# Optimization experiments

Hardware: AMD Instinct MI355X
Metric: run time of the kernel (lower is better)

Reference implementation:

```python
import jax, jax.numpy as jnp
import numpy as np

SEQ = 2048
DIM = 2048
GROUPS = 8
GROUP_SIZE = 4
DQK = DIM // (GROUPS * GROUP_SIZE)  # 64 (also dim_v)


def _glorot(key, shape):
    # Faithful to source: dim_in = prod(shape[-1]) == shape[-1], so sigma = 1/sqrt(shape[-1])
    sigma = np.sqrt(2.0 / (shape[-1] + shape[-1])).astype(np.float32)
    return jax.random.normal(key, shape, dtype=jnp.float32) * sigma


def rope(x):
    """RoPE on last axis; x: [..., seq, dim]. Closed-form per-pair rotation."""
    seq, dim = x.shape[-2], x.shape[-1]
    half = dim // 2
    # angle[s, j] = s * 10000^(-2j/dim)
    inv_freq = 10000.0 ** (-2.0 * jnp.arange(half, dtype=jnp.float32) / dim)
    ang = jnp.arange(seq, dtype=jnp.float32)[:, None] * inv_freq[None, :]  # [seq, half]
    c, s = jnp.cos(ang), jnp.sin(ang)
    xp = x.reshape(*x.shape[:-1], half, 2)
    x1, x2 = xp[..., 0], xp[..., 1]
    out = jnp.stack([c * x1 - s * x2, s * x1 + c * x2], axis=-1)
    return out.reshape(x.shape)


def setup_inputs() -> dict:
    key = jax.random.key(0)
    kx, kq, kk, kv, ko = jax.random.split(key, 5)
    return {
        "x": jax.random.normal(kx, (SEQ, DIM), dtype=jnp.float32),
        "w_query": _glorot(kq, (GROUPS, GROUP_SIZE, DIM, DQK)),
        "w_key": _glorot(kk, (GROUPS, DIM, DQK)),
        "w_value": _glorot(kv, (GROUPS, DIM, DQK)),
        "w_out": _glorot(ko, (GROUPS, GROUP_SIZE, DQK, DIM)),
    }


def reference(x, w_query, w_key, w_value, w_out):
    seq = x.shape[0]
    dqk = w_query.shape[-1]
    # projections: g=groups, h=group_size (query heads per group)
    q = rope(jnp.einsum('sd,ghdk->ghsk', x, w_query))  # [g,h,seq,dqk]
    k = rope(jnp.einsum('sd,gdk->gsk', x, w_key))      # [g,seq,dqk]
    v = jnp.einsum('sd,gdv->gsv', x, w_value)          # [g,seq,dv]
    scores = jnp.einsum('ghsk,gtk->ghst', q, k) / jnp.sqrt(jnp.float32(dqk))
    causal = jnp.tril(jnp.ones((seq, seq), dtype=bool))  # log(tril(ones)) == 0 / -inf
    scores = jnp.where(causal, scores, -jnp.inf)
    probs = jax.nn.softmax(scores, axis=-1)
    o = jnp.einsum('ghst,gtv->ghsv', probs, v)
    # per-head out-proj then sum over (g, h)
    return jnp.einsum('ghsv,ghvd->sd', o, w_out)
```

## Files before the change

### kernel.cpp

```cpp
#include <hip/hip_runtime.h>
#include <hip/hip_bf16.h>

#define SEQ 2048
#define DIMM 2048
#define NQH 32
#define NKVH 8
#define HD 64

typedef _Float16 half8 __attribute__((ext_vector_type(8)));
typedef float f32x4 __attribute__((ext_vector_type(4)));
typedef __fp16 fp16raw2 __attribute__((ext_vector_type(2)));
using fp16 = _Float16;

typedef __attribute__((address_space(1))) unsigned int ga_u32;
typedef __attribute__((address_space(3))) unsigned int ls_u32;

__device__ __forceinline__ void gll16(const void* g, void* l) {
    __builtin_amdgcn_global_load_lds((const ga_u32*)g, (ls_u32*)l, 16, 0, 0);
}

__global__ void prep_kernel(const float* __restrict__ x,
                            const float* __restrict__ wq, const float* __restrict__ wk,
                            const float* __restrict__ wv, const float* __restrict__ wo,
                            fp16* __restrict__ xh, fp16* __restrict__ wqkvt,
                            fp16* __restrict__ w2t) {
    __shared__ float tile[64][65];
    const int bx = blockIdx.x;
    const int t = threadIdx.x;
    if (bx < 1024) {
#pragma unroll
        for (int it = 0; it < 4; it++) {
            int i = bx * 4096 + it * 1024 + t * 4;
            float4 v = *reinterpret_cast<const float4*>(x + i);
            fp16* o = xh + i;
            o[0] = (fp16)v.x; o[1] = (fp16)v.y; o[2] = (fp16)v.z; o[3] = (fp16)v.w;
        }
    } else if (bx < 2560) {
        const int zi = bx - 1024;
        const int z = zi >> 5;
        const int r0 = (zi & 31) * 64;
        const float* inh = (z < 32) ? wq + (size_t)z * SEQ * HD
                                    : (z < 40) ? wk + (size_t)(z - 32) * SEQ * HD
                                               : wv + (size_t)(z - 40) * SEQ * HD;
        fp16* outh = wqkvt + (size_t)z * HD * SEQ;
#pragma unroll
        for (int i = 0; i < 16; i++) {
            int idx = i * 256 + t;
            int r = idx >> 6, c = idx & 63;
            tile[r][c] = inh[(size_t)(r0 + r) * HD + c];
        }
        __syncthreads();
#pragma unroll
        for (int i = 0; i < 16; i++) {
            int idx = i * 256 + t;
            int cc = idx >> 6, rr = idx & 63;
            outh[(size_t)cc * SEQ + r0 + rr] = (fp16)tile[rr][cc];
        }
    } else {
        const int zi = bx - 2560;
        const int r0 = (zi >> 5) * 64, c0 = (zi & 31) * 64;
#pragma unroll
        for (int i = 0; i < 16; i++) {
            int idx = i * 256 + t;
            int r = idx >> 6, c = idx & 63;
            tile[r][c] = wo[(size_t)(r0 + r) * 2048 + c0 + c];
        }
        __syncthreads();
#pragma unroll
        for (int i = 0; i < 16; i++) {
            int idx = i * 256 + t;
            int cc = idx >> 6, rr = idx & 63;
            w2t[(size_t)(c0 + cc) * 2048 + r0 + rr] = (fp16)tile[rr][cc];
        }
    }
}

__global__ void rope_vt_kernel(const fp16* __restrict__ proj, fp16* __restrict__ qb,
                               fp16* __restrict__ kb, fp16* __restrict__ vtb) {
    __shared__ fp16 tile[64][72];
    const int bx = blockIdx.x;
    if (bx < 10240) {
        int tid = bx * 256 + threadIdx.x;
        int pair = tid & 31;
        int s = (tid >> 5) & 2047;
        int head = tid >> 16;
        const fp16* src = proj + (size_t)s * 3072 + head * HD + 2 * pair;
        float x1 = (float)src[0];
        float x2 = (float)src[1];
        float invf = expf(-((float)pair / 32.0f) * 9.210340371976184f);
        float ang = (float)s * invf;
        float sn, cs;
        sincosf(ang, &sn, &cs);
        float o1 = cs * x1 - sn * x2;
        float o2 = sn * x1 + cs * x2;
        fp16* dst;
        if (head < NQH) {
            o1 *= 0.18033688011112042f;
            o2 *= 0.18033688011112042f;
            dst = qb + ((size_t)head * SEQ + s) * HD + 2 * pair;
        } else {
            dst = kb + ((size_t)(head - NQH) * SEQ + s) * HD + 2 * pair;
        }
        dst[0] = (fp16)o1;
        dst[1] = (fp16)o2;
    } else {
        const int idx = bx - 10240;
        const int g = idx >> 5;
        const int s0 = (idx & 31) * 64;
        const int t = threadIdx.x;
#pragma unroll
        for (int i = 0; i < 16; i++) {
            int id2 = i * 256 + t;
            int r = id2 >> 6, c = id2 & 63;
            tile[r][c] = proj[(size_t)(s0 + r) * 3072 + 2560 + g * HD + c];
        }
        __syncthreads();
#pragma unroll
        for (int i = 0; i < 16; i++) {
            int id2 = i * 256 + t;
            int cc = id2 >> 6, rr = id2 & 63;
            vtb[((size_t)g * HD + cc) * SEQ + s0 + rr] = tile[rr][cc];
        }
    }
}

template <int BM, int BN, int WF32>
__global__ __launch_bounds__(256) void gemm_tpl(
    const fp16* __restrict__ A, const fp16* __restrict__ Bt, void* __restrict__ Cout, int Nout) {
    __shared__ fp16 As[2][BM][64];
    __shared__ fp16 Bs[2][BN][64];
    const int t = threadIdx.x;
    const int m0 = blockIdx.x * BM, n0 = blockIdx.y * BN;
    const int wid = t >> 6, lane = t & 63;
    const int wm = (wid >> 1) * (BM / 2), wn = (wid & 1) * (BN / 2);
    const int lr = lane & 15, lg = lane >> 4;
    constexpr int MR = BM / 32, NR = BN / 32;
    f32x4 acc[MR][NR] = {};
    auto stage_ = [&](int kt, int b) {
#pragma unroll
        for (int s = t; s < BM * 8; s += 256) {
            int row = s >> 3, ch = s & 7;
            int lch = ch ^ (row & 7);
            gll16(A + (size_t)(m0 + row) * 2048 + (kt << 6) + lch * 8,
                  (char*)&As[b][0][0] + s * 16);
        }
#pragma unroll
        for (int s = t; s < BN * 8; s += 256) {
            int row = s >> 3, ch = s & 7;
            int lch = ch ^ (row & 7);
            gll16(Bt + (size_t)(n0 + row) * 2048 + (kt << 6) + lch * 8,
                  (char*)&Bs[b][0][0] + s * 16);
        }
    };
    stage_(0, 0);
    __syncthreads();
    for (int kt = 0; kt < 32; ++kt) {
        const int cur = kt & 1;
        if (kt + 1 < 32) stage_(kt + 1, cur ^ 1);
#pragma unroll
        for (int kk = 0; kk < 2; kk++) {
            half8 af[MR], bfv[NR];
#pragma unroll
            for (int m = 0; m < MR; m++) {
                int row = wm + m * 16 + lr;
                af[m] = *(const half8*)((const char*)&As[cur][row][0] +
                                        (((kk * 4 + lg) ^ (row & 7)) * 16));
            }
#pragma unroll
            for (int n = 0; n < NR; n++) {
                int row = wn + n * 16 + lr;
                bfv[n] = *(const half8*)((const char*)&Bs[cur][row][0] +
                                         (((kk * 4 + lg) ^ (row & 7)) * 16));
            }
            __builtin_amdgcn_s_setprio(1);
#pragma unroll
            for (int m = 0; m < MR; m++)
#pragma unroll
                for (int n = 0; n < NR; n++)
                    acc[m][n] = __builtin_amdgcn_mfma_f32_16x16x32_f16(af[m], bfv[n], acc[m][n], 0, 0, 0);
            __builtin_amdgcn_s_setprio(0);
        }
        __syncthreads();
    }
#pragma unroll
    for (int m = 0; m < MR; m++)
#pragma unroll
        for (int n = 0; n < NR; n++)
#pragma unroll
            for (int r = 0; r < 4; r++) {
                int row = m0 + wm + m * 16 + lg * 4 + r;
                int col = n0 + wn + n * 16 + lr;
                if (WF32)
                    ((float*)Cout)[(size_t)row * Nout + col] = acc[m][n][r];
                else
                    ((fp16*)Cout)[(size_t)row * Nout + col] = (fp16)acc[m][n][r];
            }
}

__global__ __launch_bounds__(256) void attn_kernel(
    const fp16* __restrict__ qb, const fp16* __restrict__ kb,
    const fp16* __restrict__ vt, fp16* __restrict__ o_all) {
    __shared__ fp16 Kb[2][64][64];
    __shared__ fp16 Vb[2][64][64];
    __shared__ fp16 P[4][16][64];
    const int t = threadIdx.x, wid = t >> 6, lane = t & 63;
    const int bx = blockIdx.x;
    const int grp = bx >> 5;
    const int a = grp & 7;
    const int sel = grp >> 3;
    const int qt = (sel == 0) ? (31 - a) : (sel == 1) ? (8 + a) : (sel == 2) ? (23 - a) : a;
    const int head = bx & 31;
    const int g = head >> 2;
    const int lr = lane & 15, lg = lane >> 4;
    const fp16* qh = qb + (size_t)head * SEQ * HD;
    const fp16* kh = kb + (size_t)g * SEQ * HD;
    const fp16* vh = vt + (size_t)g * HD * SEQ;
    const int srow = lane >> 3, schunk = lane & 7;
    const int qr0 = qt * 64 + wid * 16;
    char* pb = (char*)&P[wid][0][0];

    half8 aq0 = *reinterpret_cast<const half8*>(qh + (size_t)(qr0 + lr) * HD + lg * 8);
    half8 aq1 = *reinterpret_cast<const half8*>(qh + (size_t)(qr0 + lr) * HD + 32 + lg * 8);
    f32x4 o[4] = {};
    float m_ = -1e30f, lsum_ = 0.0f;
    const int nt = qt + 1;

    auto stage = [&](int kt, int b) {
        const int kv0 = kt << 6;
#pragma unroll
        for (int i = 0; i < 2; ++i) {
            int row = wid * 16 + i * 8 + srow;
            int sw = (schunk ^ srow) * 8;
            gll16(kh + (size_t)(kv0 + row) * HD + sw, &Kb[b][wid * 16 + i * 8][0]);
            gll16(vh + (size_t)row * SEQ + kv0 + sw, &Vb[b][wid * 16 + i * 8][0]);
        }
    };

    stage(0, 0);
    __syncthreads();
    for (int tt = 0; tt < nt; ++tt) {
        const int cur = tt & 1;
        if (tt + 1 < nt) stage(tt + 1, cur ^ 1);
        const int kv0 = tt << 6;
        f32x4 sc[4];
        __builtin_amdgcn_s_setprio(1);
#pragma unroll
        for (int f = 0; f < 4; ++f) {
            int row = f * 16 + lr;
            const char* kbp = (const char*)&Kb[cur][row][0];
            half8 b0 = *(const half8*)(kbp + (((lg) ^ (row & 7)) * 16));
            half8 b1 = *(const half8*)(kbp + (((4 + lg) ^ (row & 7)) * 16));
            f32x4 s = {};
            s = __builtin_amdgcn_mfma_f32_16x16x32_f16(b0, aq0, s, 0, 0, 0);
            s = __builtin_amdgcn_mfma_f32_16x16x32_f16(b1, aq1, s, 0, 0, 0);
            sc[f] = s;
        }
        __builtin_amdgcn_s_setprio(0);
        if (tt == qt) {
            const int q = qr0 + lr;
#pragma unroll
            for (int f = 0; f < 4; f++)
#pragma unroll
                for (int r = 0; r < 4; r++) {
                    int kv = kv0 + f * 16 + lg * 4 + r;
                    if (kv > q) sc[f][r] = -1e30f;
                }
        }
        float lmax = sc[0][0];
#pragma unroll
        for (int f = 0; f < 4; f++)
#pragma unroll
            for (int r = 0; r < 4; r++) lmax = fmaxf(lmax, sc[f][r]);
        if (!__all(lmax <= m_ + 11.0f)) {
            float v = lmax;
            v = fmaxf(v, __shfl_xor(v, 16));
            v = fmaxf(v, __shfl_xor(v, 32));
            float mn = fmaxf(m_, v);
            float alpha = exp2f(m_ - mn);
            m_ = mn;
            lsum_ *= alpha;
            float al[4];
#pragma unroll
            for (int r = 0; r < 4; r++) al[r] = __shfl(alpha, lg * 4 + r);
#pragma unroll
            for (int vf = 0; vf < 4; vf++)
#pragma unroll
                for (int r = 0; r < 4; r++) o[vf][r] *= al[r];
        }
#pragma unroll
        for (int f = 0; f < 4; f++) {
            float p0 = exp2f(sc[f][0] - m_);
            float p1 = exp2f(sc[f][1] - m_);
            float p2 = exp2f(sc[f][2] - m_);
            float p3 = exp2f(sc[f][3] - m_);
            lsum_ += (p0 + p1) + (p2 + p3);
            fp16raw2 k0 = __builtin_amdgcn_cvt_pkrtz(p0, p1);
            fp16raw2 k1 = __builtin_amdgcn_cvt_pkrtz(p2, p3);
            uint2 w;
            w.x = __builtin_bit_cast(unsigned int, k0);
            w.y = __builtin_bit_cast(unsigned int, k1);
            *(uint2*)(pb + lr * 128 + ((f * 32 + lg * 8) ^ ((lr & 7) << 4))) = w;
        }
        __builtin_amdgcn_s_setprio(1);
#pragma unroll
        for (int h = 0; h < 2; h++) {
            half8 pa = *(const half8*)(pb + lr * 128 + (((h * 4 + lg) ^ (lr & 7)) * 16));
#pragma unroll
            for (int vf = 0; vf < 4; vf++) {
                int d = vf * 16 + lr;
                int xo = ((h * 4 + lg) ^ (d & 7)) * 16;
                half8 bv = *(const half8*)((const char*)&Vb[cur][d][0] + xo);
                o[vf] = __builtin_amdgcn_mfma_f32_16x16x32_f16(pa, bv, o[vf], 0, 0, 0);
            }
        }
        __builtin_amdgcn_s_setprio(0);
        __syncthreads();
    }
    lsum_ += __shfl_xor(lsum_, 16);
    lsum_ += __shfl_xor(lsum_, 32);
    float li[4];
#pragma unroll
    for (int r = 0; r < 4; r++) li[r] = 1.0f / __shfl(lsum_, lg * 4 + r);
#pragma unroll
    for (int vf = 0; vf < 4; vf++)
#pragma unroll
        for (int r = 0; r < 4; r++) {
            float v = o[vf][r] * li[r];
            o_all[(size_t)(qr0 + lg * 4 + r) * 2048 + head * 64 + vf * 16 + lr] = (fp16)v;
        }
}

extern "C" void kernel_launch(void* const* d_in, const int* in_sizes, int n_in,
                              void* d_out, int out_size, void* d_ws, size_t ws_size,
                              hipStream_t stream) {
    const float* x  = (const float*)d_in[0];
    const float* wq = (const float*)d_in[1];
    const float* wk = (const float*)d_in[2];
    const float* wv = (const float*)d_in[3];
    const float* wo = (const float*)d_in[4];
    float* out = (float*)d_out;
    char* ws = (char*)d_ws;

    fp16* xh    = (fp16*)(ws);
    fp16* wqkvt = (fp16*)(ws + ((size_t)8 << 20));
    fp16* proj  = (fp16*)(ws + ((size_t)20 << 20));
    fp16* o_all = proj;
    fp16* w2t   = (fp16*)(ws + ((size_t)32 << 20));
    fp16* qbuf  = (fp16*)(ws + ((size_t)40 << 20));
    fp16* kbuf  = (fp16*)(ws + ((size_t)48 << 20));
    fp16* vtb   = (fp16*)(ws + ((size_t)50 << 20));

    prep_kernel<<<dim3(3584), 256, 0, stream>>>(x, wq, wk, wv, wo, xh, wqkvt, w2t);
    gemm_tpl<64, 128, 0><<<dim3(32, 24), 256, 0, stream>>>(xh, wqkvt, proj, 3072);
    rope_vt_kernel<<<dim3(10496), 256, 0, stream>>>(proj, qbuf, kbuf, vtb);
    attn_kernel<<<dim3(1024), 256, 0, stream>>>(qbuf, kbuf, vtb, o_all);
    gemm_tpl<64, 128, 1><<<dim3(32, 16), 256, 0, stream>>>(o_all, w2t, out, 2048);
}
```

Baseline: 133.8 us.

## Fuse RoPE, Q scaling and V transpose into the QKV projection GEMM epilogue

Replaces the separate QKV GEMM plus rope/transpose kernel with one GEMM whose epilogue applies RoPE (using a lane shuffle to get the paired element), the query scale, and an LDS-staged transpose of V written straight into the attention input buffers. This removes one kernel launch and the round trip of the intermediate projection buffer through global memory. The cost is per-element sincos work in the GEMM epilogue and scattered 2-byte stores for Q/K.

```diff
diff --git a/kernel.cpp b/kernel.cpp
--- a/kernel.cpp
+++ b/kernel.cpp
@@ -75,51 +75,106 @@
     }
 }
 
-__global__ void rope_vt_kernel(const fp16* __restrict__ proj, fp16* __restrict__ qb,
-                               fp16* __restrict__ kb, fp16* __restrict__ vtb) {
-    __shared__ fp16 tile[64][72];
-    const int bx = blockIdx.x;
-    if (bx < 10240) {
-        int tid = bx * 256 + threadIdx.x;
-        int pair = tid & 31;
-        int s = (tid >> 5) & 2047;
-        int head = tid >> 16;
-        const fp16* src = proj + (size_t)s * 3072 + head * HD + 2 * pair;
-        float x1 = (float)src[0];
-        float x2 = (float)src[1];
-        float invf = expf(-((float)pair / 32.0f) * 9.210340371976184f);
-        float ang = (float)s * invf;
-        float sn, cs;
-        sincosf(ang, &sn, &cs);
-        float o1 = cs * x1 - sn * x2;
-        float o2 = sn * x1 + cs * x2;
-        fp16* dst;
-        if (head < NQH) {
-            o1 *= 0.18033688011112042f;
-            o2 *= 0.18033688011112042f;
-            dst = qb + ((size_t)head * SEQ + s) * HD + 2 * pair;
-        } else {
-            dst = kb + ((size_t)(head - NQH) * SEQ + s) * HD + 2 * pair;
-        }
-        dst[0] = (fp16)o1;
-        dst[1] = (fp16)o2;
+__global__ __launch_bounds__(256) void gemm_qkv_fused(
+    const fp16* __restrict__ A, const fp16* __restrict__ Bt,
+    fp16* __restrict__ qb, fp16* __restrict__ kb, fp16* __restrict__ vtb) {
+    __shared__ fp16 As[2][64][64];
+    __shared__ fp16 Bs[2][128][64];
+    const int t = threadIdx.x;
+    const int m0 = blockIdx.x * 64, n0 = blockIdx.y * 128;
+    const int wid = t >> 6, lane = t & 63;
+    const int wm = (wid >> 1) * 32, wn = (wid & 1) * 64;
+    const int lr = lane & 15, lg = lane >> 4;
+    f32x4 acc[2][4] = {};
+    auto stage_ = [&](int kt, int b) {
+#pragma unroll
+        for (int s = t; s < 512; s += 256) {
+            int row = s >> 3, ch = s & 7;
+            int lch = ch ^ (row & 7);
+            gll16(A + (size_t)(m0 + row) * 2048 + (kt << 6) + lch * 8,
+                  (char*)&As[b][0][0] + s * 16);
+        }
+#pragma unroll
+        for (int s = t; s < 1024; s += 256) {
+            int row = s >> 3, ch = s & 7;
+            int lch = ch ^ (row & 7);
+            gll16(Bt + (size_t)(n0 + row) * 2048 + (kt << 6) + lch * 8,
+                  (char*)&Bs[b][0][0] + s * 16);
+        }
+    };
+    stage_(0, 0);
+    __syncthreads();
+    for (int kt = 0; kt < 32; ++kt) {
+        const int cur = kt & 1;
+        if (kt + 1 < 32) stage_(kt + 1, cur ^ 1);
+#pragma unroll
+        for (int kk = 0; kk < 2; kk++) {
+            half8 af[2], bfv[4];
+#pragma unroll
+            for (int m = 0; m < 2; m++) {
+                int row = wm + m * 16 + lr;
+                af[m] = *(const half8*)((const char*)&As[cur][row][0] +
+                                        (((kk * 4 + lg) ^ (row & 7)) * 16));
+            }
+#pragma unroll
+            for (int n = 0; n < 4; n++) {
+                int row = wn + n * 16 + lr;
+                bfv[n] = *(const half8*)((const char*)&Bs[cur][row][0] +
+                                         (((kk * 4 + lg) ^ (row & 7)) * 16));
+            }
+            __builtin_amdgcn_s_setprio(1);
+#pragma unroll
+            for (int m = 0; m < 2; m++)
+#pragma unroll
+                for (int n = 0; n < 4; n++)
+                    acc[m][n] = __builtin_amdgcn_mfma_f32_16x16x32_f16(af[m], bfv[n], acc[m][n], 0, 0, 0);
+            __builtin_amdgcn_s_setprio(0);
+        }
+        __syncthreads();
+    }
+    const int head0 = blockIdx.y * 2;
+    if (head0 < 40) {
+        const int head = head0 + (wid & 1);
+        const float qscale = (head0 < 32) ? 0.18033688011112042f : 1.0f;
+        fp16* outp = (head0 < 32) ? qb + (size_t)head * SEQ * HD
+                                  : kb + (size_t)(head - 32) * SEQ * HD;
+#pragma unroll
+        for (int n = 0; n < 4; n++) {
+            int c = n * 16 + lr;
+            float invf = expf(-0.28782313662425572f * (float)(c >> 1));
+#pragma unroll
+            for (int m = 0; m < 2; m++)
+#pragma unroll
+                for (int r = 0; r < 4; r++) {
+                    int s = m0 + wm + m * 16 + lg * 4 + r;
+                    float val = acc[m][n][r];
+                    float pv = __shfl_xor(val, 1);
+                    float sn, cs;
+                    sincosf((float)s * invf, &sn, &cs);
+                    float o = (c & 1) ? (sn * pv + cs * val) : (cs * val - sn * pv);
+                    outp[(size_t)s * HD + c] = (fp16)(o * qscale);
+                }
+        }
     } else {
-        const int idx = bx - 10240;
-        const int g = idx >> 5;
-        const int s0 = (idx & 31) * 64;
-        const int t = threadIdx.x;
+        fp16* T = (fp16*)&Bs[0][0][0];
+#pragma unroll
+        for (int n = 0; n < 4; n++)
+#pragma unroll
+            for (int m = 0; m < 2; m++)
+#pragma unroll
+                for (int r = 0; r < 4; r++) {
+                    int c = wn + n * 16 + lr;
+                    int s = wm + m * 16 + lg * 4 + r;
+                    T[c * 68 + s] = (fp16)acc[m][n][r];
+                }
+        __syncthreads();
+        const int g0 = head0 - 40;
 #pragma unroll
         for (int i = 0; i < 16; i++) {
-            int id2 = i * 256 + t;
-            int r = id2 >> 6, c = id2 & 63;
-            tile[r][c] = proj[(size_t)(s0 + r) * 3072 + 2560 + g * HD + c];
-        }
-        __syncthreads();
-#pragma unroll
-        for (int i = 0; i < 16; i++) {
-            int id2 = i * 256 + t;
-            int cc = id2 >> 6, rr = id2 & 63;
-            vtb[((size_t)g * HD + cc) * SEQ + s0 + rr] = tile[rr][cc];
+            int idx = i * 256 + t;
+            int c = idx >> 5, sp = (idx & 31) * 2;
+            unsigned v = *(const unsigned*)&T[c * 68 + sp];
+            *(unsigned*)(vtb + ((size_t)(g0 + (c >> 6)) * 64 + (c & 63)) * SEQ + m0 + sp) = v;
         }
     }
 }
@@ -343,16 +398,14 @@
 
     fp16* xh    = (fp16*)(ws);
     fp16* wqkvt = (fp16*)(ws + ((size_t)8 << 20));
-    fp16* proj  = (fp16*)(ws + ((size_t)20 << 20));
-    fp16* o_all = proj;
-    fp16* w2t   = (fp16*)(ws + ((size_t)32 << 20));
-    fp16* qbuf  = (fp16*)(ws + ((size_t)40 << 20));
-    fp16* kbuf  = (fp16*)(ws + ((size_t)48 << 20));
-    fp16* vtb   = (fp16*)(ws + ((size_t)50 << 20));
+    fp16* o_all = (fp16*)(ws + ((size_t)20 << 20));
+    fp16* w2t   = (fp16*)(ws + ((size_t)28 << 20));
+    fp16* qbuf  = (fp16*)(ws + ((size_t)36 << 20));
+    fp16* kbuf  = (fp16*)(ws + ((size_t)44 << 20));
+    fp16* vtb   = (fp16*)(ws + ((size_t)46 << 20));
 
     prep_kernel<<<dim3(3584), 256, 0, stream>>>(x, wq, wk, wv, wo, xh, wqkvt, w2t);
-    gemm_tpl<64, 128, 0><<<dim3(32, 24), 256, 0, stream>>>(xh, wqkvt, proj, 3072);
-    rope_vt_kernel<<<dim3(10496), 256, 0, stream>>>(proj, qbuf, kbuf, vtb);
+    gemm_qkv_fused<<<dim3(32, 24), 256, 0, stream>>>(xh, wqkvt, qbuf, kbuf, vtb);
     attn_kernel<<<dim3(1024), 256, 0, stream>>>(qbuf, kbuf, vtb, o_all);
     gemm_tpl<64, 128, 1><<<dim3(32, 16), 256, 0, stream>>>(o_all, w2t, out, 2048);
 }
```

Result: faster. 130.3 us (-2.6%).
